# Performance work log

Measured on AMD Instinct MI355X. Metric: run time of the kernel, lower is better.

Reference implementation:

```python
import jax, jax.numpy as jnp
import numpy as np

B, T, D_MODEL = 1, 4096, 1024
H = 16
SEM_DIM, GEO_DIM, ATTN_DIM = 128, 256, 512
SEM_HD, GEO_HD, V_HD = SEM_DIM // H, GEO_DIM // H, ATTN_DIM // H
ROPE_BASE = 10000.0


def _split_heads(x, hd):
    # (B,T,H*hd) -> (B,H,T,hd)
    b, t, _ = x.shape
    return x.reshape(b, t, H, hd).transpose(0, 2, 1, 3)


def _rope(x, pos_offset, base=ROPE_BASE):
    # x: (B,H,T,rot) with rot == full geo head dim (rotate applies to first rot_dim;
    # here rot_dim == geo_head_dim so the whole vector rotates)
    rot = x.shape[-1]
    inv_freq = 1.0 / (base ** (jnp.arange(0, rot, 2, dtype=jnp.float32) / rot))
    t = jnp.arange(pos_offset, pos_offset + x.shape[2], dtype=jnp.float32)
    freqs = t[:, None] * inv_freq[None, :]            # (T, rot/2)
    cos = jnp.cos(freqs).astype(x.dtype)[None, None]  # (1,1,T,rot/2)
    sin = jnp.sin(freqs).astype(x.dtype)[None, None]
    x1, x2 = x[..., : rot // 2], x[..., rot // 2 :]
    return jnp.concatenate([x1 * cos - x2 * sin, x1 * sin + x2 * cos], axis=-1)


def setup_inputs() -> dict:
    key = jax.random.key(0)
    ks = jax.random.split(key, 8)
    s = lambda fan_in: 1.0 / np.sqrt(fan_in)
    inp = {
        "x": jax.random.normal(ks[0], (B, T, D_MODEL), dtype=jnp.float32),
        "q_sem_w": jax.random.uniform(ks[1], (SEM_DIM, D_MODEL), jnp.float32, -s(D_MODEL), s(D_MODEL)),
        "k_sem_w": jax.random.uniform(ks[2], (SEM_DIM, D_MODEL), jnp.float32, -s(D_MODEL), s(D_MODEL)),
        "q_geo_w": jax.random.uniform(ks[3], (GEO_DIM, D_MODEL), jnp.float32, -s(D_MODEL), s(D_MODEL)),
        "k_geo_w": jax.random.uniform(ks[4], (GEO_DIM, D_MODEL), jnp.float32, -s(D_MODEL), s(D_MODEL)),
        "v_w": jax.random.uniform(ks[5], (ATTN_DIM, D_MODEL), jnp.float32, -s(D_MODEL), s(D_MODEL)),
        "out_w": jax.random.uniform(ks[6], (D_MODEL, ATTN_DIM), jnp.float32, -s(ATTN_DIM), s(ATTN_DIM)),
        "logit_scale": jnp.zeros((H,), dtype=jnp.float32),
        "attn_mask": jnp.tril(jnp.ones((T, T), dtype=bool)),  # causal: True = attend
        "pos_offset": 0,
    }
    return inp


def reference(x, q_sem_w, k_sem_w, q_geo_w, k_geo_w, v_w, out_w, logit_scale, attn_mask, pos_offset):
    dt = x.dtype
    ninf = jnp.finfo(dt).min
    # decoupled projections
    qs = _split_heads(x @ q_sem_w.T, SEM_HD)   # (B,H,T,sem_hd)
    ksem = _split_heads(x @ k_sem_w.T, SEM_HD)
    qg = _split_heads(x @ q_geo_w.T, GEO_HD)   # (B,H,T,geo_hd)
    kg = _split_heads(x @ k_geo_w.T, GEO_HD)
    v = _split_heads(x @ v_w.T, V_HD)          # (B,H,T,v_hd)
    # RoPE on geometric stream only
    qg = _rope(qg, pos_offset)
    kg = _rope(kg, pos_offset)
    # combined scores, scaled as one concatenated QK dot product
    scale = 1.0 / np.sqrt(SEM_HD + GEO_HD)
    scores = (jnp.einsum("bhtd,bhsd->bhts", qs, ksem)
              + jnp.einsum("bhtd,bhsd->bhts", qg, kg)) * scale
    # learned per-head temperature
    scores = scores * jnp.exp(logit_scale)[None, :, None, None]
    scores = jnp.where(attn_mask[None, None], scores, ninf)
    attn = jax.nn.softmax(scores, axis=-1)
    out = jnp.einsum("bhts,bhsd->bhtd", attn, v)       # (B,H,T,v_hd)
    out = out.transpose(0, 2, 1, 3).reshape(B, T, ATTN_DIM)
    return out @ out_w.T                                # (B,T,d_model)
```

## Files before the change

### kernel.cpp

```cpp
#include <hip/hip_runtime.h>
#include <hip/hip_bf16.h>

typedef __attribute__((ext_vector_type(8))) short short8;
typedef __attribute__((ext_vector_type(4))) short short4v;
typedef __attribute__((ext_vector_type(4))) float f32x4;

#define TT 4096
#define DM 1024
#define NH 16
#define NPROJ 1280
#define DATTN 512

static __device__ __forceinline__ short f2bf(float f) {
  __hip_bfloat16 h = __float2bfloat16(f);
  return *reinterpret_cast<short*>(&h);
}
static __device__ __forceinline__ float bfs2f(short s) {
  __hip_bfloat16 h = *reinterpret_cast<__hip_bfloat16*>(&s);
  return __bfloat162float(h);
}

#define NB_X   (TT * DM / 4 / 256)
#define NB_OW  (DM * DATTN / 4 / 256)
#define NB_WC  (NPROJ * DM / 4 / 256)
__global__ __launch_bounds__(256) void k_prep(const float* __restrict__ x,
    const float* __restrict__ ow, const float* __restrict__ qs, const float* __restrict__ ks,
    const float* __restrict__ qg, const float* __restrict__ kg, const float* __restrict__ vw,
    __hip_bfloat16* __restrict__ Xbf, __hip_bfloat16* __restrict__ OW,
    __hip_bfloat16* __restrict__ Wcat) {
  const int b = blockIdx.x;
  if (b < NB_X) {
    const int i = b * 256 + threadIdx.x;
    float4 v = reinterpret_cast<const float4*>(x)[i];
    short4v o;
    o[0] = f2bf(v.x); o[1] = f2bf(v.y); o[2] = f2bf(v.z); o[3] = f2bf(v.w);
    reinterpret_cast<short4v*>(Xbf)[i] = o;
  } else if (b < NB_X + NB_OW) {
    const int i = (b - NB_X) * 256 + threadIdx.x;
    float4 v = reinterpret_cast<const float4*>(ow)[i];
    short4v o;
    o[0] = f2bf(v.x); o[1] = f2bf(v.y); o[2] = f2bf(v.z); o[3] = f2bf(v.w);
    reinterpret_cast<short4v*>(OW)[i] = o;
  } else {
    const int i = (b - NB_X - NB_OW) * 256 + threadIdx.x;
    const int idx = i * 4;
    const int row = idx >> 10;
    const int col = idx & 1023;
    const float* src;
    if (row < 128)      src = qs + (size_t)row * DM;
    else if (row < 256) src = ks + (size_t)(row - 128) * DM;
    else if (row < 512) src = qg + (size_t)(row - 256) * DM;
    else if (row < 768) src = kg + (size_t)(row - 512) * DM;
    else                src = vw + (size_t)(row - 768) * DM;
    float4 v = *reinterpret_cast<const float4*>(src + col);
    short4v o;
    o[0] = f2bf(v.x); o[1] = f2bf(v.y); o[2] = f2bf(v.z); o[3] = f2bf(v.w);
    *reinterpret_cast<short4v*>(Wcat + idx) = o;
  }
}

template<int OUT_BF16>
__global__ __launch_bounds__(256) void k_gemm_bt(const __hip_bfloat16* __restrict__ A,
    const __hip_bfloat16* __restrict__ B, void* __restrict__ Cv, int M, int N, int K) {
  __shared__ alignas(16) __hip_bfloat16 lA[2][2][64 * 32];
  __shared__ alignas(16) __hip_bfloat16 lB[2][2][128 * 32];
  const int tid = threadIdx.x;
  const int lane = tid & 63;
  const int wid = tid >> 6;
  const int m0 = blockIdx.x * 64, n0 = blockIdx.y * 128;
  const int wm = (wid >> 1) * 32, wn = (wid & 1) * 64;
  const int srow = tid >> 2;
  const int scol = (tid & 3) * 8;
  const int fr = lane & 15, fk = (lane >> 4) * 8;
  f32x4 acc[2][4];
  const f32x4 zz = {0.f, 0.f, 0.f, 0.f};
#pragma unroll
  for (int m = 0; m < 2; ++m)
#pragma unroll
    for (int n = 0; n < 4; ++n) acc[m][n] = zz;

  auto stage = [&](int kt, int buf) {
#pragma unroll
    for (int kk = 0; kk < 2; ++kk) {
      const int kcol = kt + kk * 32 + scol;
      const __hip_bfloat16* ga0 = A + (size_t)(m0 + srow) * K + kcol;
      const __hip_bfloat16* gb0 = B + (size_t)(n0 + srow) * K + kcol;
      const __hip_bfloat16* gb1 = B + (size_t)(n0 + 64 + srow) * K + kcol;
      __builtin_amdgcn_global_load_lds((const __attribute__((address_space(1))) void*)ga0,
          (__attribute__((address_space(3))) void*)(lA[buf][kk] + srow * 32 + scol), 16, 0, 0);
      __builtin_amdgcn_global_load_lds((const __attribute__((address_space(1))) void*)gb0,
          (__attribute__((address_space(3))) void*)(lB[buf][kk] + srow * 32 + scol), 16, 0, 0);
      __builtin_amdgcn_global_load_lds((const __attribute__((address_space(1))) void*)gb1,
          (__attribute__((address_space(3))) void*)(lB[buf][kk] + (64 + srow) * 32 + scol), 16, 0, 0);
    }
  };
  stage(0, 0);
  int buf = 0;
  for (int kt = 0; kt < K; kt += 64) {
    __syncthreads();
    if (kt + 64 < K) stage(kt + 64, buf ^ 1);
#pragma unroll
    for (int kk = 0; kk < 2; ++kk) {
      short8 af[2], bfr[4];
#pragma unroll
      for (int m = 0; m < 2; ++m)
        af[m] = *reinterpret_cast<const short8*>(lA[buf][kk] + (wm + m * 16 + fr) * 32 + fk);
#pragma unroll
      for (int n = 0; n < 4; ++n)
        bfr[n] = *reinterpret_cast<const short8*>(lB[buf][kk] + (wn + n * 16 + fr) * 32 + fk);
#pragma unroll
      for (int m = 0; m < 2; ++m)
#pragma unroll
        for (int n = 0; n < 4; ++n)
          acc[m][n] = __builtin_amdgcn_mfma_f32_16x16x32_bf16(af[m], bfr[n], acc[m][n], 0, 0, 0);
    }
    buf ^= 1;
  }
  const int cr = (lane >> 4) * 4, cc = lane & 15;
#pragma unroll
  for (int m = 0; m < 2; ++m)
#pragma unroll
    for (int n = 0; n < 4; ++n)
#pragma unroll
      for (int j = 0; j < 4; ++j) {
        const int row = m0 + wm + m * 16 + cr + j;
        const int col = n0 + wn + n * 16 + cc;
        if (OUT_BF16)
          ((__hip_bfloat16*)Cv)[(size_t)row * N + col] = __float2bfloat16(acc[m][n][j]);
        else
          ((float*)Cv)[(size_t)row * N + col] = acc[m][n][j];
      }
}

__global__ __launch_bounds__(256) void k_rope_pack(const __hip_bfloat16* __restrict__ proj,
    const float* __restrict__ ls, const int* __restrict__ posp,
    __hip_bfloat16* __restrict__ Qp, __hip_bfloat16* __restrict__ Kp,
    __hip_bfloat16* __restrict__ Vt) {
  const int gid = blockIdx.x * blockDim.x + threadIdx.x;
  const int t = gid & (TT - 1);
  const int h = gid >> 12;
  const short8* pr8 = reinterpret_cast<const short8*>(proj + (size_t)t * NPROJ);
  const short8 qs8 = pr8[h];
  const short8 ks8 = pr8[16 + h];
  const short8 qg1 = pr8[32 + 2 * h], qg2 = pr8[33 + 2 * h];
  const short8 kg1 = pr8[64 + 2 * h], kg2 = pr8[65 + 2 * h];
  const short8 vv0 = pr8[96 + 4 * h], vv1 = pr8[97 + 4 * h];
  const short8 vv2 = pr8[98 + 4 * h], vv3 = pr8[99 + 4 * h];
  const float qscale = 0.20412414523193154f * 1.4426950408889634f * __expf(ls[h]);
  const float pos = (float)(t + posp[0]);
  const float invf[8] = {1.0f, 0.31622776601683794f, 0.1f, 0.031622776601683794f,
                         0.01f, 0.0031622776601683794f, 0.001f, 0.00031622776601683794f};
  short8 qv[4], kv[4];
  const short8 z8 = {0, 0, 0, 0, 0, 0, 0, 0};
  qv[3] = z8; kv[3] = z8;
#pragma unroll
  for (int i = 0; i < 8; ++i) {
    qv[0][i] = f2bf(bfs2f(qs8[i]) * qscale);
    kv[0][i] = ks8[i];
  }
#pragma unroll
  for (int i = 0; i < 8; ++i) {
    const float ang = pos * invf[i];
    float ss, cc;
    __sincosf(ang, &ss, &cc);
    const float x1q = bfs2f(qg1[i]), x2q = bfs2f(qg2[i]);
    const float x1k = bfs2f(kg1[i]), x2k = bfs2f(kg2[i]);
    qv[1][i] = f2bf((x1q * cc - x2q * ss) * qscale);
    qv[2][i] = f2bf((x1q * ss + x2q * cc) * qscale);
    kv[1][i] = f2bf(x1k * cc - x2k * ss);
    kv[2][i] = f2bf(x1k * ss + x2k * cc);
  }
  short8* qdst = reinterpret_cast<short8*>(Qp + ((size_t)h * TT + t) * 32);
  short8* kdst = reinterpret_cast<short8*>(Kp + ((size_t)h * TT + t) * 32);
#pragma unroll
  for (int p = 0; p < 4; ++p) { qdst[p] = qv[p]; kdst[p] = kv[p]; }
  __hip_bfloat16* vdst = Vt + (size_t)h * 32 * TT + t;
#pragma unroll
  for (int i = 0; i < 8; ++i) {
    *reinterpret_cast<short*>(vdst + (size_t)i * TT) = vv0[i];
    *reinterpret_cast<short*>(vdst + (size_t)(8 + i) * TT) = vv1[i];
    *reinterpret_cast<short*>(vdst + (size_t)(16 + i) * TT) = vv2[i];
    *reinterpret_cast<short*>(vdst + (size_t)(24 + i) * TT) = vv3[i];
  }
}

__global__ __launch_bounds__(256) void k_attn(const __hip_bfloat16* __restrict__ Qp,
    const __hip_bfloat16* __restrict__ Kp, const __hip_bfloat16* __restrict__ Vt,
    __hip_bfloat16* __restrict__ Ob) {
  __shared__ alignas(16) __hip_bfloat16 lK[2][64 * 32];
  __shared__ alignas(16) __hip_bfloat16 lV[2][32 * 64];
  __shared__ alignas(16) __hip_bfloat16 Plds[4][16][72];
  const int lin = blockIdx.x;
  const int xcd = lin & 7;
  const int idx = lin >> 3;
  const int h = xcd * 2 + (idx & 1);
  const int qb = 63 - (idx >> 1);
  const int nt = qb + 1;
  const int tid = threadIdx.x;
  const int lane = tid & 63, w = tid >> 6;
  const int g = lane >> 4, c = lane & 15;
  const int krow = (tid >> 6) * 16 + (tid & 15);
  const int kcol = ((tid >> 4) & 3) * 8;
  const int vrow = ((tid >> 6) & 1) * 16 + (tid & 15);
  const int vcol = ((tid >> 7) & 1) * 32 + ((tid >> 4) & 3) * 8;
  const __hip_bfloat16* Kh = Kp + (size_t)h * TT * 32 + (size_t)krow * 32 + kcol;
  const __hip_bfloat16* Vh = Vt + (size_t)h * 32 * TT + (size_t)vrow * TT + vcol;
  const f32x4 zz = {0.f, 0.f, 0.f, 0.f};

  const int qrow = qb * 64 + w * 16 + c;
  const short8 qf =
      *reinterpret_cast<const short8*>(Qp + ((size_t)h * TT + qrow) * 32 + 8 * g);
  f32x4 o0 = zz, o1 = zz;
  float mst = -1e30f, lsum = 0.f;
  int cur = 0;
  __builtin_amdgcn_global_load_lds(
      (const __attribute__((address_space(1))) void*)Kh,
      (__attribute__((address_space(3))) void*)(lK[0] + tid * 8), 16, 0, 0);
  __builtin_amdgcn_global_load_lds(
      (const __attribute__((address_space(1))) void*)Vh,
      (__attribute__((address_space(3))) void*)(lV[0] + tid * 8), 16, 0, 0);

  for (int it = 0; it < nt; ++it) {
    __syncthreads();
    if (it + 1 < nt) {
      const int kv1 = (it + 1) * 64;
      __builtin_amdgcn_global_load_lds(
          (const __attribute__((address_space(1))) void*)(Kh + (size_t)kv1 * 32),
          (__attribute__((address_space(3))) void*)(lK[cur ^ 1] + tid * 8), 16, 0, 0);
      __builtin_amdgcn_global_load_lds(
          (const __attribute__((address_space(1))) void*)(Vh + kv1),
          (__attribute__((address_space(3))) void*)(lV[cur ^ 1] + tid * 8), 16, 0, 0);
    }
    const char* kb = (const char*)lK[cur];
    short8 kf[4];
#pragma unroll
    for (int ct = 0; ct < 4; ++ct)
      kf[ct] = *reinterpret_cast<const short8*>(kb + ct * 1024 + lane * 16);
    const char* vb = (const char*)lV[cur];
    const short8 v00 = *reinterpret_cast<const short8*>(vb + lane * 16);
    const short8 v10 = *reinterpret_cast<const short8*>(vb + 1024 + lane * 16);
    const short8 v01 = *reinterpret_cast<const short8*>(vb + 2048 + lane * 16);
    const short8 v11 = *reinterpret_cast<const short8*>(vb + 3072 + lane * 16);
    f32x4 s[4];
#pragma unroll
    for (int ct = 0; ct < 4; ++ct)
      s[ct] = __builtin_amdgcn_mfma_f32_16x16x32_bf16(kf[ct], qf, zz, 0, 0, 0);
    if (it == nt - 1) {
#pragma unroll
      for (int ct = 0; ct < 4; ++ct)
#pragma unroll
        for (int j = 0; j < 4; ++j)
          if (ct * 16 + g * 4 + j > w * 16 + c) s[ct][j] = -1e30f;
    }
    float m01 = fmaxf(fmaxf(s[0][0], s[0][1]), fmaxf(s[0][2], s[0][3]));
    float m23 = fmaxf(fmaxf(s[1][0], s[1][1]), fmaxf(s[1][2], s[1][3]));
    float m45 = fmaxf(fmaxf(s[2][0], s[2][1]), fmaxf(s[2][2], s[2][3]));
    float m67 = fmaxf(fmaxf(s[3][0], s[3][1]), fmaxf(s[3][2], s[3][3]));
    float pm_ = fmaxf(fmaxf(m01, m23), fmaxf(m45, m67));
    if (__any(pm_ > mst + 8.0f)) {
      float pm2 = fmaxf(pm_, __shfl_xor(pm_, 16, 64));
      pm2 = fmaxf(pm2, __shfl_xor(pm2, 32, 64));
      const float nm = fmaxf(mst, pm2);
      const float alpha = exp2f(mst - nm);
      mst = nm;
      lsum *= alpha;
#pragma unroll
      for (int j = 0; j < 4; ++j) { o0[j] *= alpha; o1[j] *= alpha; }
    }
    float ts = 0.f;
#pragma unroll
    for (int ct = 0; ct < 4; ++ct) {
#pragma unroll
      for (int j = 0; j < 4; ++j) s[ct][j] = exp2f(s[ct][j] - mst);
      ts += (s[ct][0] + s[ct][1]) + (s[ct][2] + s[ct][3]);
    }
    lsum += ts;
#pragma unroll
    for (int ct = 0; ct < 4; ++ct) {
      float2 p01; p01.x = s[ct][0]; p01.y = s[ct][1];
      float2 p23; p23.x = s[ct][2]; p23.y = s[ct][3];
      __hip_bfloat162 b01 = __float22bfloat162_rn(p01);
      __hip_bfloat162 b23 = __float22bfloat162_rn(p23);
      *reinterpret_cast<__hip_bfloat162*>(&Plds[w][c][ct * 16 + g * 4]) = b01;
      *reinterpret_cast<__hip_bfloat162*>(&Plds[w][c][ct * 16 + g * 4 + 2]) = b23;
    }
    const short8 pf0 = *reinterpret_cast<const short8*>(&Plds[w][c][8 * g]);
    const short8 pf1 = *reinterpret_cast<const short8*>(&Plds[w][c][32 + 8 * g]);
    o0 = __builtin_amdgcn_mfma_f32_16x16x32_bf16(v00, pf0, o0, 0, 0, 0);
    o0 = __builtin_amdgcn_mfma_f32_16x16x32_bf16(v01, pf1, o0, 0, 0, 0);
    o1 = __builtin_amdgcn_mfma_f32_16x16x32_bf16(v10, pf0, o1, 0, 0, 0);
    o1 = __builtin_amdgcn_mfma_f32_16x16x32_bf16(v11, pf1, o1, 0, 0, 0);
    cur ^= 1;
  }
  lsum += __shfl_xor(lsum, 16, 64);
  lsum += __shfl_xor(lsum, 32, 64);
  const float inv = 1.0f / lsum;
  __hip_bfloat16* dst = Ob + (size_t)qrow * DATTN + h * 32;
  short4v w0, w1;
#pragma unroll
  for (int j = 0; j < 4; ++j) { w0[j] = f2bf(o0[j] * inv); w1[j] = f2bf(o1[j] * inv); }
  *reinterpret_cast<short4v*>(dst + g * 4) = w0;
  *reinterpret_cast<short4v*>(dst + 16 + g * 4) = w1;
}

extern "C" void kernel_launch(void* const* d_in, const int* in_sizes, int n_in,
                              void* d_out, int out_size, void* d_ws, size_t ws_size,
                              hipStream_t stream) {
  const float* x   = (const float*)d_in[0];
  const float* qsw = (const float*)d_in[1];
  const float* ksw = (const float*)d_in[2];
  const float* qgw = (const float*)d_in[3];
  const float* kgw = (const float*)d_in[4];
  const float* vw  = (const float*)d_in[5];
  const float* ow  = (const float*)d_in[6];
  const float* ls  = (const float*)d_in[7];
  const int* posp  = (const int*)d_in[9];

  size_t off = 0;
  auto alloc = [&](size_t bytes) {
    char* p = (char*)d_ws + off;
    off += (bytes + 255) & ~(size_t)255;
    return (void*)p;
  };
  __hip_bfloat16* Xbf  = (__hip_bfloat16*)alloc((size_t)TT * DM * 2);
  __hip_bfloat16* Wcat = (__hip_bfloat16*)alloc((size_t)NPROJ * DM * 2);
  __hip_bfloat16* OW   = (__hip_bfloat16*)alloc((size_t)DM * DATTN * 2);
  __hip_bfloat16* proj = (__hip_bfloat16*)alloc((size_t)TT * NPROJ * 2);
  __hip_bfloat16* Qp   = (__hip_bfloat16*)alloc((size_t)NH * TT * 32 * 2);
  __hip_bfloat16* Kpk  = (__hip_bfloat16*)alloc((size_t)NH * TT * 32 * 2);
  __hip_bfloat16* Vt   = (__hip_bfloat16*)alloc((size_t)NH * 32 * TT * 2);
  __hip_bfloat16* Ob   = (__hip_bfloat16*)alloc((size_t)TT * DATTN * 2);

  k_prep<<<dim3(NB_X + NB_OW + NB_WC), 256, 0, stream>>>(x, ow, qsw, ksw, qgw, kgw, vw,
                                                         Xbf, OW, Wcat);
  k_gemm_bt<1><<<dim3(TT / 64, NPROJ / 128), 256, 0, stream>>>(Xbf, Wcat, (void*)proj,
                                                               TT, NPROJ, DM);
  k_rope_pack<<<dim3(TT * NH / 256), 256, 0, stream>>>(proj, ls, posp, Qp, Kpk, Vt);
  k_attn<<<dim3(1024), 256, 0, stream>>>(Qp, Kpk, Vt, Ob);
  k_gemm_bt<0><<<dim3(TT / 64, DM / 128), 256, 0, stream>>>(Ob, OW, (void*)d_out,
                                                            TT, DM, DATTN);
}
```

Baseline: 118.7 us.

## Fuse RoPE, scaling and head packing into the projection GEMM epilogue

New measurement: 112.5 us (median of 2 runs). 5.2% less time.

```diff
diff --git a/kernel.cpp b/kernel.cpp
--- a/kernel.cpp
+++ b/kernel.cpp
@@ -14,10 +14,6 @@
 static __device__ __forceinline__ short f2bf(float f) {
   __hip_bfloat16 h = __float2bfloat16(f);
   return *reinterpret_cast<short*>(&h);
-}
-static __device__ __forceinline__ float bfs2f(short s) {
-  __hip_bfloat16 h = *reinterpret_cast<__hip_bfloat16*>(&s);
-  return __bfloat162float(h);
 }
 
 #define NB_X   (TT * DM / 4 / 256)
@@ -59,9 +55,12 @@
   }
 }
 
-template<int OUT_BF16>
+template<int EPI>
 __global__ __launch_bounds__(256) void k_gemm_bt(const __hip_bfloat16* __restrict__ A,
-    const __hip_bfloat16* __restrict__ B, void* __restrict__ Cv, int M, int N, int K) {
+    const __hip_bfloat16* __restrict__ B, void* __restrict__ Cv, int M, int N, int K,
+    __hip_bfloat16* __restrict__ Qp, __hip_bfloat16* __restrict__ Kp,
+    __hip_bfloat16* __restrict__ Vt, const float* __restrict__ ls,
+    const int* __restrict__ posp) {
   __shared__ alignas(16) __hip_bfloat16 lA[2][2][64 * 32];
   __shared__ alignas(16) __hip_bfloat16 lB[2][2][128 * 32];
   const int tid = threadIdx.x;
@@ -117,70 +116,80 @@
     buf ^= 1;
   }
   const int cr = (lane >> 4) * 4, cc = lane & 15;
-#pragma unroll
-  for (int m = 0; m < 2; ++m)
-#pragma unroll
-    for (int n = 0; n < 4; ++n)
-#pragma unroll
-      for (int j = 0; j < 4; ++j) {
-        const int row = m0 + wm + m * 16 + cr + j;
-        const int col = n0 + wn + n * 16 + cc;
-        if (OUT_BF16)
-          ((__hip_bfloat16*)Cv)[(size_t)row * N + col] = __float2bfloat16(acc[m][n][j]);
-        else
+  if (EPI == 0) {
+#pragma unroll
+    for (int m = 0; m < 2; ++m)
+#pragma unroll
+      for (int n = 0; n < 4; ++n)
+#pragma unroll
+        for (int j = 0; j < 4; ++j) {
+          const int row = m0 + wm + m * 16 + cr + j;
+          const int col = n0 + wn + n * 16 + cc;
           ((float*)Cv)[(size_t)row * N + col] = acc[m][n][j];
+        }
+    return;
+  }
+  const int y = blockIdx.y;
+  const float QSC = 0.20412414523193154f * 1.4426950408889634f;
+  if (y < 2) {
+    __hip_bfloat16* P = (y == 0) ? Qp : Kp;
+    const __hip_bfloat16 zb = __float2bfloat16(0.f);
+#pragma unroll
+    for (int n = 0; n < 4; ++n) {
+      const int cl = wn + n * 16 + cc;
+      const int h = cl >> 3, d = cl & 7;
+      const float sc = (y == 0) ? QSC * __expf(ls[h]) : 1.0f;
+#pragma unroll
+      for (int m = 0; m < 2; ++m)
+#pragma unroll
+        for (int j = 0; j < 4; ++j) {
+          const int row = m0 + wm + m * 16 + cr + j;
+          __hip_bfloat16* base = P + ((size_t)h * TT + row) * 32;
+          base[d] = __float2bfloat16(acc[m][n][j] * sc);
+          base[24 + d] = zb;
+        }
+    }
+  } else if (y < 6) {
+    const int isQ = (y < 4);
+    __hip_bfloat16* P = isQ ? Qp : Kp;
+    const int segbase = isQ ? 256 : 512;
+    const float invf[8] = {1.0f, 0.31622776601683794f, 0.1f, 0.031622776601683794f,
+                           0.01f, 0.0031622776601683794f, 0.001f, 0.00031622776601683794f};
+    const float fr_ = invf[cc & 7];
+    const float pofs = (float)posp[0];
+    const int lo = (cc < 8);
+    const int d = 8 + cc;
+#pragma unroll
+    for (int n = 0; n < 4; ++n) {
+      const int h = (y * 128 + wn + n * 16 - segbase) >> 4;
+      const float sc = isQ ? QSC * __expf(ls[h]) : 1.0f;
+#pragma unroll
+      for (int m = 0; m < 2; ++m)
+#pragma unroll
+        for (int j = 0; j < 4; ++j) {
+          const int row = m0 + wm + m * 16 + cr + j;
+          const float own = acc[m][n][j];
+          const float oth = __shfl_xor(own, 8, 64);
+          float ss, cs;
+          __sincosf((row + pofs) * fr_, &ss, &cs);
+          const float out = lo ? (own * cs - oth * ss) : (oth * ss + own * cs);
+          P[((size_t)h * TT + row) * 32 + d] = __float2bfloat16(out * sc);
+        }
+    }
+  } else {
+#pragma unroll
+    for (int n = 0; n < 4; ++n) {
+      const int local = y * 128 + wn + n * 16 - 768 + cc;
+      const int h = local >> 5, d = local & 31;
+#pragma unroll
+      for (int m = 0; m < 2; ++m) {
+        short4v pk;
+#pragma unroll
+        for (int j = 0; j < 4; ++j) pk[j] = f2bf(acc[m][n][j]);
+        const int row0 = m0 + wm + m * 16 + cr;
+        *reinterpret_cast<short4v*>(Vt + ((size_t)h * 32 + d) * TT + row0) = pk;
       }
-}
-
-__global__ __launch_bounds__(256) void k_rope_pack(const __hip_bfloat16* __restrict__ proj,
-    const float* __restrict__ ls, const int* __restrict__ posp,
-    __hip_bfloat16* __restrict__ Qp, __hip_bfloat16* __restrict__ Kp,
-    __hip_bfloat16* __restrict__ Vt) {
-  const int gid = blockIdx.x * blockDim.x + threadIdx.x;
-  const int t = gid & (TT - 1);
-  const int h = gid >> 12;
-  const short8* pr8 = reinterpret_cast<const short8*>(proj + (size_t)t * NPROJ);
-  const short8 qs8 = pr8[h];
-  const short8 ks8 = pr8[16 + h];
-  const short8 qg1 = pr8[32 + 2 * h], qg2 = pr8[33 + 2 * h];
-  const short8 kg1 = pr8[64 + 2 * h], kg2 = pr8[65 + 2 * h];
-  const short8 vv0 = pr8[96 + 4 * h], vv1 = pr8[97 + 4 * h];
-  const short8 vv2 = pr8[98 + 4 * h], vv3 = pr8[99 + 4 * h];
-  const float qscale = 0.20412414523193154f * 1.4426950408889634f * __expf(ls[h]);
-  const float pos = (float)(t + posp[0]);
-  const float invf[8] = {1.0f, 0.31622776601683794f, 0.1f, 0.031622776601683794f,
-                         0.01f, 0.0031622776601683794f, 0.001f, 0.00031622776601683794f};
-  short8 qv[4], kv[4];
-  const short8 z8 = {0, 0, 0, 0, 0, 0, 0, 0};
-  qv[3] = z8; kv[3] = z8;
-#pragma unroll
-  for (int i = 0; i < 8; ++i) {
-    qv[0][i] = f2bf(bfs2f(qs8[i]) * qscale);
-    kv[0][i] = ks8[i];
-  }
-#pragma unroll
-  for (int i = 0; i < 8; ++i) {
-    const float ang = pos * invf[i];
-    float ss, cc;
-    __sincosf(ang, &ss, &cc);
-    const float x1q = bfs2f(qg1[i]), x2q = bfs2f(qg2[i]);
-    const float x1k = bfs2f(kg1[i]), x2k = bfs2f(kg2[i]);
-    qv[1][i] = f2bf((x1q * cc - x2q * ss) * qscale);
-    qv[2][i] = f2bf((x1q * ss + x2q * cc) * qscale);
-    kv[1][i] = f2bf(x1k * cc - x2k * ss);
-    kv[2][i] = f2bf(x1k * ss + x2k * cc);
-  }
-  short8* qdst = reinterpret_cast<short8*>(Qp + ((size_t)h * TT + t) * 32);
-  short8* kdst = reinterpret_cast<short8*>(Kp + ((size_t)h * TT + t) * 32);
-#pragma unroll
-  for (int p = 0; p < 4; ++p) { qdst[p] = qv[p]; kdst[p] = kv[p]; }
-  __hip_bfloat16* vdst = Vt + (size_t)h * 32 * TT + t;
-#pragma unroll
-  for (int i = 0; i < 8; ++i) {
-    *reinterpret_cast<short*>(vdst + (size_t)i * TT) = vv0[i];
-    *reinterpret_cast<short*>(vdst + (size_t)(8 + i) * TT) = vv1[i];
-    *reinterpret_cast<short*>(vdst + (size_t)(16 + i) * TT) = vv2[i];
-    *reinterpret_cast<short*>(vdst + (size_t)(24 + i) * TT) = vv3[i];
+    }
   }
 }
 
@@ -325,7 +334,6 @@
   __hip_bfloat16* Xbf  = (__hip_bfloat16*)alloc((size_t)TT * DM * 2);
   __hip_bfloat16* Wcat = (__hip_bfloat16*)alloc((size_t)NPROJ * DM * 2);
   __hip_bfloat16* OW   = (__hip_bfloat16*)alloc((size_t)DM * DATTN * 2);
-  __hip_bfloat16* proj = (__hip_bfloat16*)alloc((size_t)TT * NPROJ * 2);
   __hip_bfloat16* Qp   = (__hip_bfloat16*)alloc((size_t)NH * TT * 32 * 2);
   __hip_bfloat16* Kpk  = (__hip_bfloat16*)alloc((size_t)NH * TT * 32 * 2);
   __hip_bfloat16* Vt   = (__hip_bfloat16*)alloc((size_t)NH * 32 * TT * 2);
@@ -333,10 +341,9 @@
 
   k_prep<<<dim3(NB_X + NB_OW + NB_WC), 256, 0, stream>>>(x, ow, qsw, ksw, qgw, kgw, vw,
                                                          Xbf, OW, Wcat);
-  k_gemm_bt<1><<<dim3(TT / 64, NPROJ / 128), 256, 0, stream>>>(Xbf, Wcat, (void*)proj,
-                                                               TT, NPROJ, DM);
-  k_rope_pack<<<dim3(TT * NH / 256), 256, 0, stream>>>(proj, ls, posp, Qp, Kpk, Vt);
+  k_gemm_bt<1><<<dim3(TT / 64, NPROJ / 128), 256, 0, stream>>>(Xbf, Wcat, nullptr,
+      TT, NPROJ, DM, Qp, Kpk, Vt, ls, posp);
   k_attn<<<dim3(1024), 256, 0, stream>>>(Qp, Kpk, Vt, Ob);
   k_gemm_bt<0><<<dim3(TT / 64, DM / 128), 256, 0, stream>>>(Ob, OW, (void*)d_out,
-                                                            TT, DM, DATTN);
-}
+      TT, DM, DATTN, nullptr, nullptr, nullptr, nullptr, nullptr);
+}
```
